# Kernel tuning notes

Hardware: AMD Instinct MI355X
Metric: run time of the kernel (lower is better)

Reference implementation:

```python
import jax, jax.numpy as jnp
import numpy as np

HIDDEN = 2048
NUM_HEADS = 16
HEAD_DIM = 128
WINDOW = 1024
ROPE_THETA = 10000.0
B, L = 1, 4096


def setup_inputs() -> dict:
    key = jax.random.key(0)
    k0, k1, k2, k3, k4 = jax.random.split(key, 5)
    s = 1.0 / np.sqrt(HIDDEN)
    return {
        "hidden_states": jax.random.normal(k0, (B, L, HIDDEN), dtype=jnp.float32),
        "wq": jax.random.normal(k1, (HIDDEN, NUM_HEADS * HEAD_DIM), dtype=jnp.float32) * s,
        "wk": jax.random.normal(k2, (HIDDEN, NUM_HEADS * HEAD_DIM), dtype=jnp.float32) * s,
        "wv": jax.random.normal(k3, (HIDDEN, NUM_HEADS * HEAD_DIM), dtype=jnp.float32) * s,
        "wo": jax.random.normal(k4, (NUM_HEADS * HEAD_DIM, HIDDEN), dtype=jnp.float32) * s,
    }


def _apply_rotary(x, cos, sin):
    # x: [B, H, L, D]; cos/sin: [L, D/2]
    d2 = x.shape[-1] // 2
    x1, x2 = x[..., :d2], x[..., d2:]
    return jnp.concatenate([x1 * cos - x2 * sin, x2 * cos + x1 * sin], axis=-1)


def reference(hidden_states, wq, wk, wv, wo):
    Bsz, Ln, _ = hidden_states.shape
    dtype = hidden_states.dtype
    scale = HEAD_DIM ** (-0.5)

    def split_heads(x):
        return x.reshape(Bsz, Ln, NUM_HEADS, HEAD_DIM).transpose(0, 2, 1, 3)

    q = split_heads(hidden_states @ wq)
    k = split_heads(hidden_states @ wk)
    v = split_heads(hidden_states @ wv)

    inv_freq = 1.0 / (ROPE_THETA ** (jnp.arange(0, HEAD_DIM, 2, dtype=jnp.float32) / HEAD_DIM))
    pos = jnp.arange(Ln, dtype=jnp.float32)
    freqs = pos[:, None] * inv_freq[None, :]  # [L, D/2]
    cos = jnp.cos(freqs).astype(dtype)
    sin = jnp.sin(freqs).astype(dtype)

    q = _apply_rotary(q, cos, sin)
    k = _apply_rotary(k, cos, sin)

    q_pos = jnp.arange(Ln)[:, None]
    k_pos = jnp.arange(Ln)[None, :]
    valid = (k_pos > q_pos - WINDOW) & (k_pos <= q_pos)  # [L, L]
    neg = jnp.finfo(dtype).min

    attn = jnp.einsum("bhqd,bhkd->bhqk", q, k) * scale
    attn = jnp.where(valid, attn, neg)
    attn = jax.nn.softmax(attn, axis=-1)
    out = jnp.einsum("bhqk,bhkd->bhqd", attn, v)
    out = out.transpose(0, 2, 1, 3).reshape(Bsz, Ln, NUM_HEADS * HEAD_DIM)
    return out @ wo
```

## Files before the change

### kernel.cpp

```cpp
#include <hip/hip_runtime.h>
#include <cstdint>
#include <cstddef>

typedef unsigned short u16;
typedef __bf16 bf16x8 __attribute__((ext_vector_type(8)));
typedef float f32x4 __attribute__((ext_vector_type(4)));
typedef unsigned short u16x8 __attribute__((ext_vector_type(8)));

#define SEQ 4096
#define HID 2048
#define NH 16
#define HD 128
#define WIN 1024

__device__ __forceinline__ float bf2f(u16 u) {
  union { unsigned int i; float f; } v; v.i = ((unsigned int)u) << 16; return v.f;
}
__device__ __forceinline__ u16 f2bf(float f) {
  union { float f; unsigned int i; } v; v.f = f;
  unsigned int r = v.i + 0x7FFFu + ((v.i >> 16) & 1u);
  return (u16)(r >> 16);
}
__device__ __forceinline__ u16 f2bf_rne(float f) {
  union { __bf16 b; u16 u; } v; v.b = (__bf16)f; return v.u;
}
__device__ __forceinline__ float exp2a(float x) {
  float r; asm("v_exp_f32 %0, %1" : "=v"(r) : "v"(x)); return r;
}
template<int L2R>
__device__ __forceinline__ unsigned swz(unsigned o) { return o ^ (((o >> L2R) & 7u) << 4); }

__device__ __forceinline__ void gload_lds16(const u16* g, u16* l) {
  __builtin_amdgcn_global_load_lds((const __attribute__((address_space(1))) void*)g,
                                   (__attribute__((address_space(3))) void*)l, 16, 0, 0);
}


__global__ void cast_f32_bf16(const float* __restrict__ in, u16* __restrict__ out, int n4) {
  int i = blockIdx.x * blockDim.x + threadIdx.x;
  if (i < n4) {
    float4 v = ((const float4*)in)[i];
    union { u16 u[4]; unsigned long long ll; } r;
    r.u[0] = f2bf(v.x); r.u[1] = f2bf(v.y); r.u[2] = f2bf(v.z); r.u[3] = f2bf(v.w);
    ((unsigned long long*)out)[i] = r.ll;
  }
}

__global__ void transpose_cast(const float* __restrict__ W, u16* __restrict__ Wt) {
  __shared__ float t[32][33];
  const int tx = threadIdx.x & 31, ty = threadIdx.x >> 5;
  const int x0 = blockIdx.x * 32, y0 = blockIdx.y * 32;
#pragma unroll
  for (int i = 0; i < 4; ++i)
    t[ty + i * 8][tx] = W[(size_t)(y0 + ty + i * 8) * HID + x0 + tx];
  __syncthreads();
#pragma unroll
  for (int i = 0; i < 4; ++i)
    Wt[(size_t)(x0 + ty + i * 8) * HID + y0 + tx] = f2bf(t[tx][ty + i * 8]);
}

__global__ void rope_table(float* __restrict__ ctab, float* __restrict__ stab) {
  int idx = blockIdx.x * blockDim.x + threadIdx.x;
  int pos = idx >> 6, i = idx & 63;
  float invf = expf(-(float)i * 0.14391156831212787f);
  float ang = (float)pos * invf;
  float s, c;
  sincosf(ang, &s, &c);
  ctab[idx] = c; stab[idx] = s;
}

__global__ void rope_apply(u16* __restrict__ Qb, u16* __restrict__ Kb,
                           const float* __restrict__ ctab, const float* __restrict__ stab) {
  int idx = blockIdx.x * blockDim.x + threadIdx.x;
  int pos = idx >> 10;
  int rem = idx & 1023;
  int h = rem >> 6, i = rem & 63;
  size_t base = (size_t)pos * HID + h * HD + i;
  float c = ctab[(pos << 6) + i], s = stab[(pos << 6) + i];
  float q1 = bf2f(Qb[base]), q2 = bf2f(Qb[base + 64]);
  Qb[base] = f2bf(q1 * c - q2 * s);
  Qb[base + 64] = f2bf(q2 * c + q1 * s);
  float k1 = bf2f(Kb[base]), k2 = bf2f(Kb[base + 64]);
  Kb[base] = f2bf(k1 * c - k2 * s);
  Kb[base + 64] = f2bf(k2 * c + k1 * s);
}


template<bool OUT_F32>
__device__ __forceinline__ void gemm_body(const u16* __restrict__ A, const u16* __restrict__ Bt,
                                          void* __restrict__ C, int brow, int bcol,
                                          u16 (&ldsA)[2][8192], u16 (&ldsB)[2][8192]) {
  const int lane = threadIdx.x & 63;
  const int wv = threadIdx.x >> 6;
  const int wr = wv >> 1, wc = wv & 1;
  const int K = HID, N = HID;

  const f32x4 zero = {0.f, 0.f, 0.f, 0.f};
  f32x4 acc[4][4];
#pragma unroll
  for (int m = 0; m < 4; ++m)
#pragma unroll
    for (int n = 0; n < 4; ++n) acc[m][n] = zero;

  auto stage = [&](int buf, int kt) {
    const int k0 = kt * 64;
#pragma unroll
    for (int i = 0; i < 4; ++i) {
      unsigned o = ((unsigned)(wv * 4 + i) * 64 + (unsigned)lane) * 16u;
      unsigned r = o >> 7;
      unsigned cb = swz<7>(o) & 127u;
      const size_t gcol = (size_t)k0 + (cb >> 1);
      gload_lds16(A + (size_t)(brow + r) * K + gcol, &ldsA[buf][(wv * 4 + i) * 512]);
      gload_lds16(Bt + (size_t)(bcol + r) * K + gcol, &ldsB[buf][(wv * 4 + i) * 512]);
    }
  };

  stage(0, 0);
  __syncthreads();
  int buf = 0;
  const int nt = K / 64;
  for (int kt = 0; kt < nt; ++kt) {
    if (kt + 1 < nt) stage(buf ^ 1, kt + 1);
    __builtin_amdgcn_s_setprio(1);
#pragma unroll
    for (int s = 0; s < 2; ++s) {
      const unsigned kb = (unsigned)(s * 64 + ((lane >> 4) & 3) * 16);
      bf16x8 af[4], bfv[4];
#pragma unroll
      for (int m = 0; m < 4; ++m) {
        unsigned row = wr * 64 + m * 16 + (lane & 15);
        af[m] = *(const bf16x8*)((const char*)&ldsA[buf][0] + swz<7>(row * 128 + kb));
      }
#pragma unroll
      for (int n = 0; n < 4; ++n) {
        unsigned row = wc * 64 + n * 16 + (lane & 15);
        bfv[n] = *(const bf16x8*)((const char*)&ldsB[buf][0] + swz<7>(row * 128 + kb));
      }
#pragma unroll
      for (int m = 0; m < 4; ++m)
#pragma unroll
        for (int n = 0; n < 4; ++n)
          acc[m][n] = __builtin_amdgcn_mfma_f32_16x16x32_bf16(af[m], bfv[n], acc[m][n], 0, 0, 0);
    }
    __builtin_amdgcn_s_setprio(0);
    __syncthreads();
    buf ^= 1;
  }

#pragma unroll
  for (int m = 0; m < 4; ++m) {
    const int rbase = brow + wr * 64 + m * 16 + ((lane >> 4) & 3) * 4;
#pragma unroll
    for (int n = 0; n < 4; ++n) {
      const int cbase = bcol + wc * 64 + n * 16 + (lane & 15);
#pragma unroll
      for (int r = 0; r < 4; ++r) {
        const size_t idx = (size_t)(rbase + r) * N + cbase;
        if (OUT_F32) ((float*)C)[idx] = acc[m][n][r];
        else ((u16*)C)[idx] = f2bf(acc[m][n][r]);
      }
    }
  }
}

__global__ __launch_bounds__(256, 2) void gemm_qkv_kernel(
    const u16* __restrict__ X, const u16* __restrict__ Wqt, const u16* __restrict__ Wkt,
    const u16* __restrict__ Wvt, u16* __restrict__ Qo, u16* __restrict__ Ko, u16* __restrict__ Vo) {
  __shared__ u16 ldsA[2][8192];
  __shared__ u16 ldsB[2][8192];
  int flat = (blockIdx.z * 32 + blockIdx.y) * 16 + blockIdx.x;
  int nf = (flat & 7) * 192 + (flat >> 3);
  int bx = nf & 15, by = (nf >> 4) & 31, bz = nf >> 9;
  const u16* Bt = (bz == 0) ? Wqt : (bz == 1) ? Wkt : Wvt;
  u16* C = (bz == 0) ? Qo : (bz == 1) ? Ko : Vo;
  gemm_body<false>(X, Bt, C, by * 128, bx * 128, ldsA, ldsB);
}

__global__ __launch_bounds__(256, 2) void gemm_out_kernel(
    const u16* __restrict__ Ob, const u16* __restrict__ Wot, float* __restrict__ out) {
  __shared__ u16 ldsA[2][8192];
  __shared__ u16 ldsB[2][8192];
  int flat = blockIdx.y * 16 + blockIdx.x;
  int nf = (flat & 7) * 64 + (flat >> 3);
  int bx = nf & 15, by = nf >> 4;
  gemm_body<true>(Ob, Wot, out, by * 128, bx * 128, ldsA, ldsB);
}


__global__ __launch_bounds__(256, 2) void attn_kernel(
    const u16* __restrict__ Q, const u16* __restrict__ K,
    const u16* __restrict__ V, u16* __restrict__ O) {
  __shared__ u16 k_lds[2][8192];
  __shared__ u16 vt_lds[2][128 * 72];
  __shared__ u16 p_lds[4][16 * 72];

  const int lane = threadIdx.x & 63;
  const int wv = threadIdx.x >> 6;
  const int g = lane >> 4;
  const int c = lane & 15;

  int flat = blockIdx.y * 64 + blockIdx.x;
  int nf = (flat & 7) * 128 + (flat >> 3);
  const int q0 = (nf & 63) * 64;
  const int h = nf >> 6;

#pragma unroll
  for (int i = 0; i < 4; ++i) {
    unsigned o = ((unsigned)(wv * 4 + i) * 64 + (unsigned)lane) * 16u;
    unsigned r = o >> 8;
    unsigned cb = swz<8>(o) & 255u;
    gload_lds16(Q + (size_t)(q0 + r) * HID + h * HD + (cb >> 1), &k_lds[0][(wv * 4 + i) * 512]);
  }
  __syncthreads();
  bf16x8 qf[4];
#pragma unroll
  for (int s = 0; s < 4; ++s) {
    unsigned row = wv * 16 + c;
    qf[s] = *(const bf16x8*)((const char*)&k_lds[0][0] + swz<8>(row * 256 + s * 64 + g * 16));
  }
  __syncthreads();

  const int t_start = (q0 >= WIN) ? (q0 - WIN) : 0;

#pragma unroll
  for (int i = 0; i < 4; ++i) {
    unsigned o = ((unsigned)(wv * 4 + i) * 64 + (unsigned)lane) * 16u;
    unsigned r = o >> 8;
    unsigned cb = swz<8>(o) & 255u;
    gload_lds16(K + (size_t)(t_start + r) * HID + h * HD + (cb >> 1), &k_lds[0][(wv * 4 + i) * 512]);
  }
  {
    const u16x8* src = (const u16x8*)(V + (size_t)(t_start + lane) * HID + h * HD + wv * 32);
#pragma unroll
    for (int it = 0; it < 4; ++it) {
      u16x8 vv = src[it];
#pragma unroll
      for (int j = 0; j < 8; ++j)
        vt_lds[0][(wv * 32 + it * 8 + j) * 72 + lane] = vv[j];
    }
  }
  __syncthreads();

  const f32x4 zero = {0.f, 0.f, 0.f, 0.f};
  float mrow[4], lrow[4];
  f32x4 oacc[8];
#pragma unroll
  for (int r = 0; r < 4; ++r) { mrow[r] = -1e30f; lrow[r] = 0.f; }
#pragma unroll
  for (int d = 0; d < 8; ++d) oacc[d] = zero;

  const float scale2 = 0.12751743f;
  int b = 0;

  for (int t0 = t_start; t0 <= q0; t0 += 64) {
    const int nb = b ^ 1;
    const bool has_next = (t0 + 64 <= q0);

    u16x8 vreg[4];
    if (has_next) {
#pragma unroll
      for (int i = 0; i < 4; ++i) {
        unsigned o = ((unsigned)(wv * 4 + i) * 64 + (unsigned)lane) * 16u;
        unsigned r = o >> 8;
        unsigned cb = swz<8>(o) & 255u;
        gload_lds16(K + (size_t)(t0 + 64 + r) * HID + h * HD + (cb >> 1),
                    &k_lds[nb][(wv * 4 + i) * 512]);
      }
      const u16x8* src = (const u16x8*)(V + (size_t)(t0 + 64 + lane) * HID + h * HD + wv * 32);
#pragma unroll
      for (int it = 0; it < 4; ++it) vreg[it] = src[it];
    }

    f32x4 sa[4];
#pragma unroll
    for (int kf = 0; kf < 4; ++kf) sa[kf] = zero;
    __builtin_amdgcn_s_setprio(1);
#pragma unroll
    for (int s = 0; s < 4; ++s) {
#pragma unroll
      for (int kf = 0; kf < 4; ++kf) {
        unsigned row = kf * 16 + c;
        bf16x8 kb = *(const bf16x8*)((const char*)&k_lds[b][0] + swz<8>(row * 256 + s * 64 + g * 16));
        sa[kf] = __builtin_amdgcn_mfma_f32_16x16x32_bf16(qf[s], kb, sa[kf], 0, 0, 0);
      }
    }
    __builtin_amdgcn_s_setprio(0);

    const int qbase = q0 + wv * 16 + g * 4;
    const bool diag = (t0 == q0);
    const bool lowm = (q0 >= WIN) && (t0 == t_start);
    if (diag) {
#pragma unroll
      for (int kf = 0; kf < 4; ++kf) {
        const int kpos = t0 + kf * 16 + c;
#pragma unroll
        for (int r = 0; r < 4; ++r) {
          float x = sa[kf][r] * scale2;
          sa[kf][r] = (kpos <= qbase + r) ? x : -1e30f;
        }
      }
    } else if (lowm) {
#pragma unroll
      for (int kf = 0; kf < 4; ++kf) {
        const int kpos = t0 + kf * 16 + c;
#pragma unroll
        for (int r = 0; r < 4; ++r) {
          float x = sa[kf][r] * scale2;
          sa[kf][r] = (kpos > qbase + r - WIN) ? x : -1e30f;
        }
      }
    } else {
#pragma unroll
      for (int kf = 0; kf < 4; ++kf)
#pragma unroll
        for (int r = 0; r < 4; ++r) sa[kf][r] *= scale2;
    }

    float tmax[4];
#pragma unroll
    for (int r = 0; r < 4; ++r)
      tmax[r] = fmaxf(fmaxf(sa[0][r], sa[1][r]), fmaxf(sa[2][r], sa[3][r]));
#pragma unroll
    for (int r = 0; r < 4; ++r)
#pragma unroll
      for (int d = 1; d < 16; d <<= 1)
        tmax[r] = fmaxf(tmax[r], __shfl_xor(tmax[r], d, 16));

    bool okl = (tmax[0] <= mrow[0] + 8.f) && (tmax[1] <= mrow[1] + 8.f) &&
               (tmax[2] <= mrow[2] + 8.f) && (tmax[3] <= mrow[3] + 8.f);
    if (!__all((int)okl)) {
#pragma unroll
      for (int r = 0; r < 4; ++r) {
        const float mn = fmaxf(mrow[r], tmax[r]);
        const float al = exp2a(mrow[r] - mn);
        mrow[r] = mn;
        lrow[r] *= al;
#pragma unroll
        for (int df = 0; df < 8; ++df) oacc[df][r] *= al;
      }
    }

    float rs[4] = {0.f, 0.f, 0.f, 0.f};
    if (diag || lowm) {
#pragma unroll
      for (int kf = 0; kf < 4; ++kf)
#pragma unroll
        for (int r = 0; r < 4; ++r) {
          const float x = sa[kf][r];
          const float p = (x < -1e29f) ? 0.f : exp2a(x - mrow[r]);
          sa[kf][r] = p; rs[r] += p;
        }
    } else {
#pragma unroll
      for (int kf = 0; kf < 4; ++kf)
#pragma unroll
        for (int r = 0; r < 4; ++r) {
          const float p = exp2a(sa[kf][r] - mrow[r]);
          sa[kf][r] = p; rs[r] += p;
        }
    }
#pragma unroll
    for (int r = 0; r < 4; ++r) {
#pragma unroll
      for (int d = 1; d < 16; d <<= 1) rs[r] += __shfl_xor(rs[r], d, 16);
      lrow[r] += rs[r];
    }

#pragma unroll
    for (int kf = 0; kf < 4; ++kf)
#pragma unroll
      for (int r = 0; r < 4; ++r)
        p_lds[wv][(g * 4 + r) * 72 + kf * 16 + c] = f2bf_rne(sa[kf][r]);

    if (has_next) {
#pragma unroll
      for (int it = 0; it < 4; ++it)
#pragma unroll
        for (int j = 0; j < 8; ++j)
          vt_lds[nb][(wv * 32 + it * 8 + j) * 72 + lane] = vreg[it][j];
    }

    asm volatile("" ::: "memory");

    __builtin_amdgcn_s_setprio(1);
#pragma unroll
    for (int s2 = 0; s2 < 2; ++s2) {
      const bf16x8 pa = *(const bf16x8*)((const char*)&p_lds[wv][0] + (c * 144 + s2 * 64 + g * 16));
#pragma unroll
      for (int df = 0; df < 8; ++df) {
        const bf16x8 vb = *(const bf16x8*)((const char*)&vt_lds[b][0] + ((df * 16 + c) * 144 + s2 * 64 + g * 16));
        oacc[df] = __builtin_amdgcn_mfma_f32_16x16x32_bf16(pa, vb, oacc[df], 0, 0, 0);
      }
    }
    __builtin_amdgcn_s_setprio(0);
    __syncthreads();
    b = nb;
  }

  float invl[4];
#pragma unroll
  for (int r = 0; r < 4; ++r) invl[r] = 1.f / lrow[r];
#pragma unroll
  for (int df = 0; df < 8; ++df)
#pragma unroll
    for (int r = 0; r < 4; ++r) {
      const int row = q0 + wv * 16 + g * 4 + r;
      const int col = h * HD + df * 16 + c;
      O[(size_t)row * HID + col] = f2bf(oacc[df][r] * invl[r]);
    }
}


extern "C" void kernel_launch(void* const* d_in, const int* in_sizes, int n_in,
                              void* d_out, int out_size, void* d_ws, size_t ws_size,
                              hipStream_t stream) {
  const float* hidden = (const float*)d_in[0];
  const float* wq = (const float*)d_in[1];
  const float* wk = (const float*)d_in[2];
  const float* wv = (const float*)d_in[3];
  const float* wo = (const float*)d_in[4];
  float* out = (float*)d_out;

  char* ws = (char*)d_ws;
  u16* Xb  = (u16*)ws;                 ws += (size_t)SEQ * HID * 2;
  u16* Wqt = (u16*)ws;                 ws += (size_t)HID * HID * 2;
  u16* Wkt = (u16*)ws;                 ws += (size_t)HID * HID * 2;
  u16* Wvt = (u16*)ws;                 ws += (size_t)HID * HID * 2;
  u16* Wot = (u16*)ws;                 ws += (size_t)HID * HID * 2;
  u16* Qb  = (u16*)ws;                 ws += (size_t)SEQ * HID * 2;
  u16* Kb  = (u16*)ws;                 ws += (size_t)SEQ * HID * 2;
  u16* Vb  = (u16*)ws;                 ws += (size_t)SEQ * HID * 2;
  u16* Ob  = (u16*)ws;                 ws += (size_t)SEQ * HID * 2;
  float* ctab = (float*)ws;            ws += (size_t)SEQ * 64 * 4;
  float* stab = (float*)ws;            ws += (size_t)SEQ * 64 * 4;

  cast_f32_bf16<<<(SEQ * HID / 4 + 255) / 256, 256, 0, stream>>>(hidden, Xb, SEQ * HID / 4);

  dim3 tg(64, 64);
  transpose_cast<<<tg, 256, 0, stream>>>(wq, Wqt);
  transpose_cast<<<tg, 256, 0, stream>>>(wk, Wkt);
  transpose_cast<<<tg, 256, 0, stream>>>(wv, Wvt);
  transpose_cast<<<tg, 256, 0, stream>>>(wo, Wot);

  rope_table<<<(SEQ * 64) / 256, 256, 0, stream>>>(ctab, stab);

  dim3 gq(HID / 128, SEQ / 128, 3);
  gemm_qkv_kernel<<<gq, 256, 0, stream>>>(Xb, Wqt, Wkt, Wvt, Qb, Kb, Vb);

  rope_apply<<<(SEQ * NH * 64) / 256, 256, 0, stream>>>(Qb, Kb, ctab, stab);

  dim3 ga(SEQ / 64, NH);
  attn_kernel<<<ga, 256, 0, stream>>>(Qb, Kb, Vb, Ob);

  dim3 go(HID / 128, SEQ / 128);
  gemm_out_kernel<<<go, 256, 0, stream>>>(Ob, Wot, out);
}
```

Measured before the change: 300.5 us.

## Widen attention blocks to 128 queries with 8 waves sharing K/V tiles

The attention kernel now processes 128 query rows per block with 8 waves (512 threads) instead of 64 rows with 4 waves, so each staged K/V tile serves twice as many queries. Per-wave compute is skipped for tiles outside that wave's causal/window range. The padded LDS layouts are replaced with XOR-swizzled layouts, and Q is loaded directly from global memory into registers. The trade-offs are extra tiles iterated per block (the window span plus 64), idle waves on tiles they skip, and a higher occupancy demand from launch_bounds(512,4).

After: 343.5 us. +14.3%, slower.

```diff
diff --git a/kernel.cpp b/kernel.cpp
--- a/kernel.cpp
+++ b/kernel.cpp
@@ -187,57 +187,65 @@
 }
 
 
-__global__ __launch_bounds__(256, 2) void attn_kernel(
+__global__ __launch_bounds__(512, 4) void attn_kernel(
     const u16* __restrict__ Q, const u16* __restrict__ K,
     const u16* __restrict__ V, u16* __restrict__ O) {
   __shared__ u16 k_lds[2][8192];
-  __shared__ u16 vt_lds[2][128 * 72];
-  __shared__ u16 p_lds[4][16 * 72];
+  __shared__ u16 vt_lds[2][8192];
+  __shared__ u16 p_lds[8][1024];
 
   const int lane = threadIdx.x & 63;
   const int wv = threadIdx.x >> 6;
   const int g = lane >> 4;
   const int c = lane & 15;
 
-  int flat = blockIdx.y * 64 + blockIdx.x;
-  int nf = (flat & 7) * 128 + (flat >> 3);
-  const int q0 = (nf & 63) * 64;
-  const int h = nf >> 6;
-
-#pragma unroll
-  for (int i = 0; i < 4; ++i) {
-    unsigned o = ((unsigned)(wv * 4 + i) * 64 + (unsigned)lane) * 16u;
-    unsigned r = o >> 8;
-    unsigned cb = swz<8>(o) & 255u;
-    gload_lds16(Q + (size_t)(q0 + r) * HID + h * HD + (cb >> 1), &k_lds[0][(wv * 4 + i) * 512]);
-  }
-  __syncthreads();
+  int flat = blockIdx.y * 32 + blockIdx.x;
+  int nf = (flat & 7) * 64 + (flat >> 3);
+  const int q0 = (nf & 31) * 128;
+  const int h = nf >> 5;
+  const int qw = q0 + wv * 16;
+
   bf16x8 qf[4];
-#pragma unroll
-  for (int s = 0; s < 4; ++s) {
-    unsigned row = wv * 16 + c;
-    qf[s] = *(const bf16x8*)((const char*)&k_lds[0][0] + swz<8>(row * 256 + s * 64 + g * 16));
-  }
-  __syncthreads();
+  {
+    const u16* qrow = Q + (size_t)(qw + c) * HID + h * HD;
+#pragma unroll
+    for (int s = 0; s < 4; ++s)
+      qf[s] = *(const bf16x8*)(qrow + s * 32 + g * 8);
+  }
 
   const int t_start = (q0 >= WIN) ? (q0 - WIN) : 0;
-
-#pragma unroll
-  for (int i = 0; i < 4; ++i) {
-    unsigned o = ((unsigned)(wv * 4 + i) * 64 + (unsigned)lane) * 16u;
-    unsigned r = o >> 8;
-    unsigned cb = swz<8>(o) & 255u;
-    gload_lds16(K + (size_t)(t_start + r) * HID + h * HD + (cb >> 1), &k_lds[0][(wv * 4 + i) * 512]);
-  }
+  const int t_end = q0 + 64;
+
+  auto stageK = [&](int buf, int t0) {
+#pragma unroll
+    for (int i = 0; i < 2; ++i) {
+      unsigned idx = (unsigned)(i * 512 + threadIdx.x);
+      unsigned o = idx * 16u;
+      unsigned r = o >> 8;
+      unsigned cb = swz<8>(o) & 255u;
+      gload_lds16(K + (size_t)(t0 + r) * HID + h * HD + (cb >> 1), &k_lds[buf][idx * 8]);
+    }
+  };
+  auto loadV = [&](int t0, u16x8* vr) {
+    const u16x8* src = (const u16x8*)(V + (size_t)(t0 + lane) * HID + h * HD + wv * 16);
+    vr[0] = src[0];
+    vr[1] = src[1];
+  };
+  auto writeVT = [&](int buf, const u16x8* vr) {
+#pragma unroll
+    for (int it = 0; it < 2; ++it)
+#pragma unroll
+      for (int j = 0; j < 8; ++j) {
+        const int d = wv * 16 + it * 8 + j;
+        vt_lds[buf][d * 64 + (lane ^ ((d & 7) << 3))] = vr[it][j];
+      }
+  };
+
   {
-    const u16x8* src = (const u16x8*)(V + (size_t)(t_start + lane) * HID + h * HD + wv * 32);
-#pragma unroll
-    for (int it = 0; it < 4; ++it) {
-      u16x8 vv = src[it];
-#pragma unroll
-      for (int j = 0; j < 8; ++j)
-        vt_lds[0][(wv * 32 + it * 8 + j) * 72 + lane] = vv[j];
-    }
+    u16x8 vr[2];
+    stageK(0, t_start);
+    loadV(t_start, vr);
+    writeVT(0, vr);
   }
   __syncthreads();
 
@@ -252,147 +260,141 @@
   const float scale2 = 0.12751743f;
   int b = 0;
 
-  for (int t0 = t_start; t0 <= q0; t0 += 64) {
+  for (int t0 = t_start; t0 <= t_end; t0 += 64) {
     const int nb = b ^ 1;
-    const bool has_next = (t0 + 64 <= q0);
-
-    u16x8 vreg[4];
+    const bool has_next = (t0 + 64 <= t_end);
+
+    u16x8 vr[2];
     if (has_next) {
-#pragma unroll
-      for (int i = 0; i < 4; ++i) {
-        unsigned o = ((unsigned)(wv * 4 + i) * 64 + (unsigned)lane) * 16u;
-        unsigned r = o >> 8;
-        unsigned cb = swz<8>(o) & 255u;
-        gload_lds16(K + (size_t)(t0 + 64 + r) * HID + h * HD + (cb >> 1),
-                    &k_lds[nb][(wv * 4 + i) * 512]);
-      }
-      const u16x8* src = (const u16x8*)(V + (size_t)(t0 + 64 + lane) * HID + h * HD + wv * 32);
-#pragma unroll
-      for (int it = 0; it < 4; ++it) vreg[it] = src[it];
-    }
-
-    f32x4 sa[4];
-#pragma unroll
-    for (int kf = 0; kf < 4; ++kf) sa[kf] = zero;
-    __builtin_amdgcn_s_setprio(1);
-#pragma unroll
-    for (int s = 0; s < 4; ++s) {
-#pragma unroll
-      for (int kf = 0; kf < 4; ++kf) {
-        unsigned row = kf * 16 + c;
-        bf16x8 kb = *(const bf16x8*)((const char*)&k_lds[b][0] + swz<8>(row * 256 + s * 64 + g * 16));
-        sa[kf] = __builtin_amdgcn_mfma_f32_16x16x32_bf16(qf[s], kb, sa[kf], 0, 0, 0);
-      }
-    }
-    __builtin_amdgcn_s_setprio(0);
-
-    const int qbase = q0 + wv * 16 + g * 4;
-    const bool diag = (t0 == q0);
-    const bool lowm = (q0 >= WIN) && (t0 == t_start);
-    if (diag) {
-#pragma unroll
-      for (int kf = 0; kf < 4; ++kf) {
-        const int kpos = t0 + kf * 16 + c;
+      stageK(nb, t0 + 64);
+      loadV(t0 + 64, vr);
+    }
+
+    const bool compute = (t0 <= qw + 15) && (t0 + 63 >= qw - (WIN - 1));
+
+    if (compute) {
+      f32x4 sa[4];
+#pragma unroll
+      for (int kf = 0; kf < 4; ++kf) sa[kf] = zero;
+      __builtin_amdgcn_s_setprio(1);
+#pragma unroll
+      for (int s = 0; s < 4; ++s) {
+#pragma unroll
+        for (int kf = 0; kf < 4; ++kf) {
+          const int row = kf * 16 + c;
+          const bf16x8 kb = *(const bf16x8*)&k_lds[b][row * 128 + ((s * 32 + g * 8) ^ ((row & 7) << 3))];
+          sa[kf] = __builtin_amdgcn_mfma_f32_16x16x32_bf16(qf[s], kb, sa[kf], 0, 0, 0);
+        }
+      }
+      __builtin_amdgcn_s_setprio(0);
+
+      const int qbase = qw + g * 4;
+      const bool causal = (t0 + 63 > qw);
+      const bool edge = (t0 < qw - (WIN - 16));
+      if (causal) {
+#pragma unroll
+        for (int kf = 0; kf < 4; ++kf) {
+          const int kpos = t0 + kf * 16 + c;
+#pragma unroll
+          for (int r = 0; r < 4; ++r) {
+            float x = sa[kf][r] * scale2;
+            sa[kf][r] = (kpos <= qbase + r) ? x : -1e30f;
+          }
+        }
+      } else if (edge) {
+#pragma unroll
+        for (int kf = 0; kf < 4; ++kf) {
+          const int kpos = t0 + kf * 16 + c;
+#pragma unroll
+          for (int r = 0; r < 4; ++r) {
+            float x = sa[kf][r] * scale2;
+            sa[kf][r] = (kpos > qbase + r - WIN) ? x : -1e30f;
+          }
+        }
+      } else {
+#pragma unroll
+        for (int kf = 0; kf < 4; ++kf)
+#pragma unroll
+          for (int r = 0; r < 4; ++r) sa[kf][r] *= scale2;
+      }
+
+      float tmax[4];
+#pragma unroll
+      for (int r = 0; r < 4; ++r)
+        tmax[r] = fmaxf(fmaxf(sa[0][r], sa[1][r]), fmaxf(sa[2][r], sa[3][r]));
+#pragma unroll
+      for (int r = 0; r < 4; ++r)
+#pragma unroll
+        for (int d = 1; d < 16; d <<= 1)
+          tmax[r] = fmaxf(tmax[r], __shfl_xor(tmax[r], d, 16));
+
+      bool okl = (tmax[0] <= mrow[0] + 8.f) && (tmax[1] <= mrow[1] + 8.f) &&
+                 (tmax[2] <= mrow[2] + 8.f) && (tmax[3] <= mrow[3] + 8.f);
+      if (!__all((int)okl)) {
 #pragma unroll
         for (int r = 0; r < 4; ++r) {
-          float x = sa[kf][r] * scale2;
-          sa[kf][r] = (kpos <= qbase + r) ? x : -1e30f;
-        }
-      }
-    } else if (lowm) {
-#pragma unroll
-      for (int kf = 0; kf < 4; ++kf) {
-        const int kpos = t0 + kf * 16 + c;
+          const float mn = fmaxf(mrow[r], tmax[r]);
+          const float al = exp2a(mrow[r] - mn);
+          mrow[r] = mn;
+          lrow[r] *= al;
+#pragma unroll
+          for (int df = 0; df < 8; ++df) oacc[df][r] *= al;
+        }
+      }
+
+      float rs[4] = {0.f, 0.f, 0.f, 0.f};
+      if (causal || edge) {
+#pragma unroll
+        for (int kf = 0; kf < 4; ++kf)
+#pragma unroll
+          for (int r = 0; r < 4; ++r) {
+            const float x = sa[kf][r];
+            const float p = (x < -1e29f) ? 0.f : exp2a(x - mrow[r]);
+            sa[kf][r] = p; rs[r] += p;
+          }
+      } else {
+#pragma unroll
+        for (int kf = 0; kf < 4; ++kf)
+#pragma unroll
+          for (int r = 0; r < 4; ++r) {
+            const float p = exp2a(sa[kf][r] - mrow[r]);
+            sa[kf][r] = p; rs[r] += p;
+          }
+      }
+#pragma unroll
+      for (int r = 0; r < 4; ++r) {
+#pragma unroll
+        for (int d = 1; d < 16; d <<= 1) rs[r] += __shfl_xor(rs[r], d, 16);
+        lrow[r] += rs[r];
+      }
+
+#pragma unroll
+      for (int kf = 0; kf < 4; ++kf)
 #pragma unroll
         for (int r = 0; r < 4; ++r) {
-          float x = sa[kf][r] * scale2;
-          sa[kf][r] = (kpos > qbase + r - WIN) ? x : -1e30f;
-        }
-      }
-    } else {
-#pragma unroll
-      for (int kf = 0; kf < 4; ++kf)
-#pragma unroll
-        for (int r = 0; r < 4; ++r) sa[kf][r] *= scale2;
-    }
-
-    float tmax[4];
-#pragma unroll
-    for (int r = 0; r < 4; ++r)
-      tmax[r] = fmaxf(fmaxf(sa[0][r], sa[1][r]), fmaxf(sa[2][r], sa[3][r]));
-#pragma unroll
-    for (int r = 0; r < 4; ++r)
-#pragma unroll
-      for (int d = 1; d < 16; d <<= 1)
-        tmax[r] = fmaxf(tmax[r], __shfl_xor(tmax[r], d, 16));
-
-    bool okl = (tmax[0] <= mrow[0] + 8.f) && (tmax[1] <= mrow[1] + 8.f) &&
-               (tmax[2] <= mrow[2] + 8.f) && (tmax[3] <= mrow[3] + 8.f);
-    if (!__all((int)okl)) {
-#pragma unroll
-      for (int r = 0; r < 4; ++r) {
-        const float mn = fmaxf(mrow[r], tmax[r]);
-        const float al = exp2a(mrow[r] - mn);
-        mrow[r] = mn;
-        lrow[r] *= al;
-#pragma unroll
-        for (int df = 0; df < 8; ++df) oacc[df][r] *= al;
-      }
-    }
-
-    float rs[4] = {0.f, 0.f, 0.f, 0.f};
-    if (diag || lowm) {
-#pragma unroll
-      for (int kf = 0; kf < 4; ++kf)
-#pragma unroll
-        for (int r = 0; r < 4; ++r) {
-          const float x = sa[kf][r];
-          const float p = (x < -1e29f) ? 0.f : exp2a(x - mrow[r]);
-          sa[kf][r] = p; rs[r] += p;
-        }
-    } else {
-#pragma unroll
-      for (int kf = 0; kf < 4; ++kf)
-#pragma unroll
-        for (int r = 0; r < 4; ++r) {
-          const float p = exp2a(sa[kf][r] - mrow[r]);
-          sa[kf][r] = p; rs[r] += p;
-        }
-    }
-#pragma unroll
-    for (int r = 0; r < 4; ++r) {
-#pragma unroll
-      for (int d = 1; d < 16; d <<= 1) rs[r] += __shfl_xor(rs[r], d, 16);
-      lrow[r] += rs[r];
-    }
-
-#pragma unroll
-    for (int kf = 0; kf < 4; ++kf)
-#pragma unroll
-      for (int r = 0; r < 4; ++r)
-        p_lds[wv][(g * 4 + r) * 72 + kf * 16 + c] = f2bf_rne(sa[kf][r]);
-
-    if (has_next) {
-#pragma unroll
-      for (int it = 0; it < 4; ++it)
-#pragma unroll
-        for (int j = 0; j < 8; ++j)
-          vt_lds[nb][(wv * 32 + it * 8 + j) * 72 + lane] = vreg[it][j];
-    }
+          const int q = g * 4 + r;
+          p_lds[wv][q * 64 + ((kf * 16 + c) ^ ((q & 7) << 3))] = f2bf_rne(sa[kf][r]);
+        }
+    }
+
+    if (has_next) writeVT(nb, vr);
 
     asm volatile("" ::: "memory");
 
-    __builtin_amdgcn_s_setprio(1);
-#pragma unroll
-    for (int s2 = 0; s2 < 2; ++s2) {
-      const bf16x8 pa = *(const bf16x8*)((const char*)&p_lds[wv][0] + (c * 144 + s2 * 64 + g * 16));
-#pragma unroll
-      for (int df = 0; df < 8; ++df) {
-        const bf16x8 vb = *(const bf16x8*)((const char*)&vt_lds[b][0] + ((df * 16 + c) * 144 + s2 * 64 + g * 16));
-        oacc[df] = __builtin_amdgcn_mfma_f32_16x16x32_bf16(pa, vb, oacc[df], 0, 0, 0);
-      }
-    }
-    __builtin_amdgcn_s_setprio(0);
+    if (compute) {
+      __builtin_amdgcn_s_setprio(1);
+#pragma unroll
+      for (int s2 = 0; s2 < 2; ++s2) {
+        const bf16x8 pa = *(const bf16x8*)&p_lds[wv][c * 64 + ((s2 * 32 + g * 8) ^ ((c & 7) << 3))];
+#pragma unroll
+        for (int df = 0; df < 8; ++df) {
+          const int row = df * 16 + c;
+          const bf16x8 vb = *(const bf16x8*)&vt_lds[b][row * 64 + ((s2 * 32 + g * 8) ^ ((row & 7) << 3))];
+          oacc[df] = __builtin_amdgcn_mfma_f32_16x16x32_bf16(pa, vb, oacc[df], 0, 0, 0);
+        }
+      }
+      __builtin_amdgcn_s_setprio(0);
+    }
     __syncthreads();
     b = nb;
   }
@@ -404,7 +406,7 @@
   for (int df = 0; df < 8; ++df)
 #pragma unroll
     for (int r = 0; r < 4; ++r) {
-      const int row = q0 + wv * 16 + g * 4 + r;
+      const int row = qw + g * 4 + r;
       const int col = h * HD + df * 16 + c;
       O[(size_t)row * HID + col] = f2bf(oacc[df][r] * invl[r]);
     }
@@ -449,8 +451,8 @@
 
   rope_apply<<<(SEQ * NH * 64) / 256, 256, 0, stream>>>(Qb, Kb, ctab, stab);
 
-  dim3 ga(SEQ / 64, NH);
-  attn_kernel<<<ga, 256, 0, stream>>>(Qb, Kb, Vb, Ob);
+  dim3 ga(SEQ / 128, NH);
+  attn_kernel<<<ga, 512, 0, stream>>>(Qb, Kb, Vb, Ob);
 
   dim3 go(HID / 128, SEQ / 128);
   gemm_out_kernel<<<go, 256, 0, stream>>>(Ob, Wot, out);
```

## Swizzle V-transpose and P LDS buffers, merge four weight transposes into one launch

Applied to the files above, without the earlier changes.

Replaces the padded stride-72 LDS layouts for the transposed V tile and the P tile with unpadded stride-64 rows that XOR-swizzle each 8-element group by the row index. The aim is to avoid bank conflicts on the scalar transposed stores and the 16-byte MFMA operand reads, and to cut LDS footprint. It also fuses the four weight transpose-cast launches into a single launch that uses a z grid dimension, removing launch overhead. The swizzled index arithmetic adds some ALU work and must match between the writes and the reads.

Result: faster. 291.4 us (-3.1%).

```diff
diff --git a/kernel.cpp b/kernel.cpp
--- a/kernel.cpp
+++ b/kernel.cpp
@@ -46,8 +46,13 @@
   }
 }
 
-__global__ void transpose_cast(const float* __restrict__ W, u16* __restrict__ Wt) {
+__global__ void transpose_cast4(const float* __restrict__ w0, const float* __restrict__ w1,
+                                const float* __restrict__ w2, const float* __restrict__ w3,
+                                u16* __restrict__ o0, u16* __restrict__ o1,
+                                u16* __restrict__ o2, u16* __restrict__ o3) {
   __shared__ float t[32][33];
+  const float* W = (blockIdx.z == 0) ? w0 : (blockIdx.z == 1) ? w1 : (blockIdx.z == 2) ? w2 : w3;
+  u16* Wt = (blockIdx.z == 0) ? o0 : (blockIdx.z == 1) ? o1 : (blockIdx.z == 2) ? o2 : o3;
   const int tx = threadIdx.x & 31, ty = threadIdx.x >> 5;
   const int x0 = blockIdx.x * 32, y0 = blockIdx.y * 32;
 #pragma unroll
@@ -191,8 +196,8 @@
     const u16* __restrict__ Q, const u16* __restrict__ K,
     const u16* __restrict__ V, u16* __restrict__ O) {
   __shared__ u16 k_lds[2][8192];
-  __shared__ u16 vt_lds[2][128 * 72];
-  __shared__ u16 p_lds[4][16 * 72];
+  __shared__ u16 vt_lds[2][8192];
+  __shared__ u16 p_lds[4][1024];
 
   const int lane = threadIdx.x & 63;
   const int wv = threadIdx.x >> 6;
@@ -235,8 +240,10 @@
     for (int it = 0; it < 4; ++it) {
       u16x8 vv = src[it];
 #pragma unroll
-      for (int j = 0; j < 8; ++j)
-        vt_lds[0][(wv * 32 + it * 8 + j) * 72 + lane] = vv[j];
+      for (int j = 0; j < 8; ++j) {
+        const int d = wv * 32 + it * 8 + j;
+        vt_lds[0][d * 64 + (lane ^ ((d & 7) << 3))] = vv[j];
+      }
     }
   }
   __syncthreads();
@@ -256,7 +263,7 @@
     const int nb = b ^ 1;
     const bool has_next = (t0 + 64 <= q0);
 
-    u16x8 vreg[4];
+    u16x8 vr[4];
     if (has_next) {
 #pragma unroll
       for (int i = 0; i < 4; ++i) {
@@ -268,7 +275,7 @@
       }
       const u16x8* src = (const u16x8*)(V + (size_t)(t0 + 64 + lane) * HID + h * HD + wv * 32);
 #pragma unroll
-      for (int it = 0; it < 4; ++it) vreg[it] = src[it];
+      for (int it = 0; it < 4; ++it) vr[it] = src[it];
     }
 
     f32x4 sa[4];
@@ -369,15 +376,19 @@
 #pragma unroll
     for (int kf = 0; kf < 4; ++kf)
 #pragma unroll
-      for (int r = 0; r < 4; ++r)
-        p_lds[wv][(g * 4 + r) * 72 + kf * 16 + c] = f2bf_rne(sa[kf][r]);
+      for (int r = 0; r < 4; ++r) {
+        const int q = g * 4 + r;
+        p_lds[wv][q * 64 + ((kf * 16 + c) ^ ((q & 7) << 3))] = f2bf_rne(sa[kf][r]);
+      }
 
     if (has_next) {
 #pragma unroll
       for (int it = 0; it < 4; ++it)
 #pragma unroll
-        for (int j = 0; j < 8; ++j)
-          vt_lds[nb][(wv * 32 + it * 8 + j) * 72 + lane] = vreg[it][j];
+        for (int j = 0; j < 8; ++j) {
+          const int d = wv * 32 + it * 8 + j;
+          vt_lds[nb][d * 64 + (lane ^ ((d & 7) << 3))] = vr[it][j];
+        }
     }
 
     asm volatile("" ::: "memory");
@@ -385,10 +396,11 @@
     __builtin_amdgcn_s_setprio(1);
 #pragma unroll
     for (int s2 = 0; s2 < 2; ++s2) {
-      const bf16x8 pa = *(const bf16x8*)((const char*)&p_lds[wv][0] + (c * 144 + s2 * 64 + g * 16));
+      const bf16x8 pa = *(const bf16x8*)&p_lds[wv][c * 64 + ((s2 * 32 + g * 8) ^ ((c & 7) << 3))];
 #pragma unroll
       for (int df = 0; df < 8; ++df) {
-        const bf16x8 vb = *(const bf16x8*)((const char*)&vt_lds[b][0] + ((df * 16 + c) * 144 + s2 * 64 + g * 16));
+        const int row = df * 16 + c;
+        const bf16x8 vb = *(const bf16x8*)&vt_lds[b][row * 64 + ((s2 * 32 + g * 8) ^ ((row & 7) << 3))];
         oacc[df] = __builtin_amdgcn_mfma_f32_16x16x32_bf16(pa, vb, oacc[df], 0, 0, 0);
       }
     }
@@ -436,11 +448,8 @@
 
   cast_f32_bf16<<<(SEQ * HID / 4 + 255) / 256, 256, 0, stream>>>(hidden, Xb, SEQ * HID / 4);
 
-  dim3 tg(64, 64);
-  transpose_cast<<<tg, 256, 0, stream>>>(wq, Wqt);
-  transpose_cast<<<tg, 256, 0, stream>>>(wk, Wkt);
-  transpose_cast<<<tg, 256, 0, stream>>>(wv, Wvt);
-  transpose_cast<<<tg, 256, 0, stream>>>(wo, Wot);
+  dim3 tg(64, 64, 4);
+  transpose_cast4<<<tg, 256, 0, stream>>>(wq, wk, wv, wo, Wqt, Wkt, Wvt, Wot);
 
   rope_table<<<(SEQ * 64) / 256, 256, 0, stream>>>(ctab, stab);
 
```
